# Performance work log

Hardware: AMD Instinct MI355X
Metric: run time of the kernel (lower is better)

The kernel has to match this reference:

```python
import jax, jax.numpy as jnp
import numpy as np

# SH constants (standard 3DGS eval_sh, degree 3)
C0 = 0.28209479177387814
C1 = 0.4886025119029199
C2 = (1.0925484305920792, -1.0925484305920792, 0.31539156525252005, -1.0925484305920792, 0.5462742152960396)
C3 = (-0.5900435899266435, 2.890611442640554, -0.4570457994644658, 0.3731763325901154, -0.4570457994644658, 1.445305721320277, -0.5900435899266435)

N_GAUSS = 4096
N_PTS = 32768
CHUNK = 4096  # math-identical to torch's 16384 chunking (pure concat of independent points)


def quat_to_rot(q):
    # q: (N,4) normalized, (w,x,y,z) as in 3DGS build_rotation
    r, x, y, z = q[:, 0], q[:, 1], q[:, 2], q[:, 3]
    R = jnp.stack([
        jnp.stack([1 - 2 * (y * y + z * z), 2 * (x * y - r * z), 2 * (x * z + r * y)], -1),
        jnp.stack([2 * (x * y + r * z), 1 - 2 * (x * x + z * z), 2 * (y * z - r * x)], -1),
        jnp.stack([2 * (x * z - r * y), 2 * (y * z + r * x), 1 - 2 * (x * x + y * y)], -1),
    ], axis=-2)  # (N,3,3)
    return R


def eval_sh3(sh, dirs):
    # sh: (N,16) scalar SH coeffs; dirs: (C,N,3) unit directions -> (C,N)
    x, y, z = dirs[..., 0], dirs[..., 1], dirs[..., 2]
    xx, yy, zz = x * x, y * y, z * z
    xy, yz, xz = x * y, y * z, x * z
    s = sh[None]  # (1,N,16)
    res = C0 * s[..., 0]
    res = res - C1 * y * s[..., 1] + C1 * z * s[..., 2] - C1 * x * s[..., 3]
    res = (res + C2[0] * xy * s[..., 4] + C2[1] * yz * s[..., 5]
           + C2[2] * (2 * zz - xx - yy) * s[..., 6]
           + C2[3] * xz * s[..., 7] + C2[4] * (xx - yy) * s[..., 8])
    res = (res + C3[0] * y * (3 * xx - yy) * s[..., 9] + C3[1] * xy * z * s[..., 10]
           + C3[2] * y * (4 * zz - xx - yy) * s[..., 11]
           + C3[3] * z * (2 * zz - 3 * xx - 3 * yy) * s[..., 12]
           + C3[4] * x * (4 * zz - xx - yy) * s[..., 13]
           + C3[5] * z * (xx - yy) * s[..., 14]
           + C3[6] * x * (xx - yy - 3 * zz) * s[..., 15])
    return res


def setup_inputs() -> dict:
    key = jax.random.key(0)
    ks = jax.random.split(key, 9)
    return {
        "network_pts": jax.random.normal(ks[0], (N_PTS, 3), jnp.float32),
        "network_view": jax.random.normal(ks[1], (N_PTS, 3), jnp.float32),
        "network_tx": jax.random.normal(ks[2], (N_PTS, 3), jnp.float32),
        "xyz": jax.random.normal(ks[3], (N_GAUSS, 3), jnp.float32),
        "sh_dc": jax.random.normal(ks[4], (N_GAUSS, 1), jnp.float32),
        "sh_rest": 0.1 * jax.random.normal(ks[5], (N_GAUSS, 15), jnp.float32),
        "scaling": jnp.float32(-3.0) + 0.2 * jax.random.normal(ks[6], (N_GAUSS, 3), jnp.float32),
        "rotation": jax.random.normal(ks[7], (N_GAUSS, 4), jnp.float32),
        "opacity_logit": jax.random.normal(ks[8], (N_GAUSS, 1), jnp.float32),
    }


def reference(network_pts, network_view, network_tx, xyz, sh_dc, sh_rest, scaling, rotation, opacity_logit):
    # activations, matching GaussianModel.setup_functions
    sh = jnp.concatenate([sh_dc, sh_rest], axis=1)            # (N,16)
    s = jnp.exp(scaling)                                      # (N,3)
    q = rotation / jnp.linalg.norm(rotation, axis=1, keepdims=True)
    R = quat_to_rot(q)                                        # (N,3,3)
    # precision = (L L^T)^{-1} with L = R diag(s)  =>  R diag(1/s^2) R^T
    prec = jnp.einsum('nij,nj,nkj->nik', R, 1.0 / (s * s), R)  # (N,3,3)
    op = jax.nn.sigmoid(opacity_logit)[:, 0]                  # (N,)

    pts = network_pts.reshape(-1, CHUNK, 3)

    def chunk_fn(p):  # p: (C,3)
        diff = p[:, None, :] - xyz[None, :, :]                # (C,N,3)
        maha = jnp.einsum('cni,nij,cnj->cn', diff, prec, diff)
        w = op[None, :] * jnp.exp(-0.5 * maha)                # (C,N)
        # dir_pp = xyz - query_point, normalized (as in get_magnitude)
        dirs = -diff / jnp.linalg.norm(diff, axis=-1, keepdims=True)
        mag = jnp.maximum(eval_sh3(sh, dirs), 0.0)            # (C,N)
        return w.sum(axis=1), (w * mag).sum(axis=1)

    opac_c, sig_c = jax.lax.map(chunk_fn, pts)
    return opac_c.reshape(-1), sig_c.reshape(-1)
```

## Files before the change

kernel.cpp:

```cpp
#include <hip/hip_runtime.h>
#include <hip/hip_bf16.h>

#define N_GAUSS 4096
#define N_PTS   32768
#define BLOCK   256
#define NSPLIT  32
#define SEGSZ   (N_GAUSS / NSPLIT)
#define NBLK_PT 128
#define GSTRIDE 28
#define NCELL   4096

#define SH_C0  0.28209479177387814f
#define SH_C1  0.4886025119029199f

#define WS_GP     0
#define WS_GHIST  114688
#define WS_CELLID 118784
#define WS_SPTS   151552
#define WS_PART   282624

__device__ __forceinline__ int cell_of(float x, float y, float z) {
    int cx = min(15, max(0, (int)((x + 3.2f) * 2.5f)));
    int cy = min(15, max(0, (int)((y + 3.2f) * 2.5f)));
    int cz = min(15, max(0, (int)((z + 3.2f) * 2.5f)));
    int ex = (cx & 1) | ((cx & 2) << 2) | ((cx & 4) << 4) | ((cx & 8) << 6);
    int ey = (cy & 1) | ((cy & 2) << 2) | ((cy & 4) << 4) | ((cy & 8) << 6);
    int ez = (cz & 1) | ((cz & 2) << 2) | ((cz & 4) << 4) | ((cz & 8) << 6);
    return ex | (ey << 1) | (ez << 2);
}

__global__ __launch_bounds__(1024) void setup_kernel(
    const float* __restrict__ pts, const float* __restrict__ xyz,
    const float* __restrict__ sh_dc, const float* __restrict__ sh_rest,
    const float* __restrict__ scaling, const float* __restrict__ rotation,
    const float* __restrict__ opl, float* __restrict__ gp,
    int* __restrict__ cellid, int* __restrict__ ghist)
{
    const int t = threadIdx.x, bx = blockIdx.x;

    if (bx > 0) {
        int g = (bx - 1) * 1024 + t;
        float s0 = scaling[3*g+0], s1 = scaling[3*g+1], s2 = scaling[3*g+2];
        float i0 = __expf(-2.0f * s0);
        float i1 = __expf(-2.0f * s1);
        float i2 = __expf(-2.0f * s2);
        float maxs2 = __expf(2.0f * fmaxf(s0, fmaxf(s1, s2)));

        float r = rotation[4*g+0], x = rotation[4*g+1];
        float y = rotation[4*g+2], z = rotation[4*g+3];
        float n = rsqrtf(r*r + x*x + y*y + z*z);
        r *= n; x *= n; y *= n; z *= n;
        float R00 = 1.f - 2.f*(y*y + z*z), R01 = 2.f*(x*y - r*z), R02 = 2.f*(x*z + r*y);
        float R10 = 2.f*(x*y + r*z), R11 = 1.f - 2.f*(x*x + z*z), R12 = 2.f*(y*z - r*x);
        float R20 = 2.f*(x*z - r*y), R21 = 2.f*(y*z + r*x), R22 = 1.f - 2.f*(x*x + y*y);

        float pxx = 0.5f*(R00*R00*i0 + R01*R01*i1 + R02*R02*i2);
        float pxy = 0.5f*(R00*R10*i0 + R01*R11*i1 + R02*R12*i2);
        float pxz = 0.5f*(R00*R20*i0 + R01*R21*i1 + R02*R22*i2);
        float pyy = 0.5f*(R10*R10*i0 + R11*R11*i1 + R12*R12*i2);
        float pyz = 0.5f*(R10*R20*i0 + R11*R21*i1 + R12*R22*i2);
        float pzz = 0.5f*(R20*R20*i0 + R21*R21*i1 + R22*R22*i2);

        float op   = 1.f / (1.f + __expf(-opl[g]));
        float lnop = __logf(op);
        float Tg   = 2.0f * maxs2 * (lnop + 16.0f);

        float* G = gp + (size_t)g * GSTRIDE;
        G[0] = xyz[3*g+0]; G[1] = xyz[3*g+1]; G[2] = xyz[3*g+2]; G[3] = Tg;
        G[4] = pxx; G[5] = pxy; G[6] = pxz; G[7] = pyy; G[8] = pyz; G[9] = pzz;
        G[10] = lnop; G[11] = 0.f;

        const float* sr = sh_rest + (size_t)g * 15;
        G[12] =  SH_C0 * sh_dc[g];
        G[13] = -SH_C1 * sr[0];
        G[14] =  SH_C1 * sr[1];
        G[15] = -SH_C1 * sr[2];
        G[16] =  1.0925484305920792f  * sr[3];
        G[17] = -1.0925484305920792f  * sr[4];
        G[18] =  0.31539156525252005f * sr[5];
        G[19] = -1.0925484305920792f  * sr[6];
        G[20] =  0.5462742152960396f  * sr[7];
        G[21] = -0.5900435899266435f  * sr[8];
        G[22] =  2.890611442640554f   * sr[9];
        G[23] = -0.4570457994644658f  * sr[10];
        G[24] =  0.3731763325901154f  * sr[11];
        G[25] = -0.4570457994644658f  * sr[12];
        G[26] =  1.445305721320277f   * sr[13];
        G[27] = -0.5900435899266435f  * sr[14];
        return;
    }

    __shared__ int s_hist[NCELL];
    __shared__ int s_scan[1024];
    #pragma unroll
    for (int i = 0; i < 4; ++i) s_hist[t + i * 1024] = 0;
    __syncthreads();
    for (int p = t; p < N_PTS; p += 1024) {
        float x = pts[3*p+0], y = pts[3*p+1], z = pts[3*p+2];
        int cell = cell_of(x, y, z);
        cellid[p] = cell;
        atomicAdd(&s_hist[cell], 1);
    }
    __syncthreads();
    int b = t * 4;
    int c0 = s_hist[b], c1 = s_hist[b+1], c2 = s_hist[b+2], c3 = s_hist[b+3];
    int s = c0 + c1 + c2 + c3;
    s_scan[t] = s;
    __syncthreads();
    for (int off = 1; off < 1024; off <<= 1) {
        int v = (t >= off) ? s_scan[t - off] : 0;
        __syncthreads();
        s_scan[t] += v;
        __syncthreads();
    }
    int excl = s_scan[t] - s;
    ghist[b]   = excl;
    ghist[b+1] = excl + c0;
    ghist[b+2] = excl + c0 + c1;
    ghist[b+3] = excl + c0 + c1 + c2;
}

__global__ __launch_bounds__(256) void scatter_kernel(
    const float* __restrict__ pts, const int* __restrict__ cellid,
    int* __restrict__ ghist, float4* __restrict__ spts)
{
    int p = blockIdx.x * 256 + threadIdx.x;
    float x = pts[3*p+0], y = pts[3*p+1], z = pts[3*p+2];
    int pos = atomicAdd(&ghist[cellid[p]], 1);
    spts[pos] = make_float4(x, y, z, __int_as_float(p));
}

__device__ __forceinline__ void eval_one(
    const float* __restrict__ G, float dx, float dy, float dz, float d2,
    float& opac, float& sig)
{
    float vx = G[4]*dx + G[5]*dy + G[6]*dz;
    float vy = G[5]*dx + G[7]*dy + G[8]*dz;
    float vz = G[6]*dx + G[8]*dy + G[9]*dz;
    float maha = dx*vx + dy*vy + dz*vz;
    float w = __expf(G[10] - maha);
    opac += w;

    if (__any(w > 1e-9f)) {
        float rinv = rsqrtf(d2);
        float x = -dx * rinv, y = -dy * rinv, z = -dz * rinv;
        float xx = x*x, yy = y*y, zz = z*z;
        float xy = x*y, yz = y*z, xz = x*z;

        float res = G[12];
        res += y * G[13];
        res += z * G[14];
        res += x * G[15];
        res += xy * G[16];
        res += yz * G[17];
        res += (3.f*zz - 1.f) * G[18];
        res += xz * G[19];
        float xxmyy = xx - yy;
        res += xxmyy * G[20];
        res += y * (3.f*xx - yy) * G[21];
        res += (xy * z) * G[22];
        float f5z1 = 5.f*zz - 1.f;
        res += y * f5z1 * G[23];
        res += z * (5.f*zz - 3.f) * G[24];
        res += x * f5z1 * G[25];
        res += z * xxmyy * G[26];
        res += x * (xxmyy - 3.f*zz) * G[27];

        sig += w * fmaxf(res, 0.f);
    }
}

__global__ __launch_bounds__(BLOCK, 4) void gauss_kernel(
    const float4* __restrict__ spts, const float* __restrict__ gp,
    float2* __restrict__ part)
{
    __shared__ float s_min[4][3], s_max[4][3];
    __shared__ int s_nact;
    __shared__ int s_act[SEGSZ];

    const int tid = threadIdx.x;
    const int pb  = blockIdx.x;
    const int seg = blockIdx.y;
    float4 P = spts[pb * 256 + tid];
    const float px = P.x, py = P.y, pz = P.z;

    float mnx = px, mxx = px, mny = py, mxy = py, mnz = pz, mxz = pz;
    #pragma unroll
    for (int off = 32; off >= 1; off >>= 1) {
        mnx = fminf(mnx, __shfl_xor(mnx, off));
        mxx = fmaxf(mxx, __shfl_xor(mxx, off));
        mny = fminf(mny, __shfl_xor(mny, off));
        mxy = fmaxf(mxy, __shfl_xor(mxy, off));
        mnz = fminf(mnz, __shfl_xor(mnz, off));
        mxz = fmaxf(mxz, __shfl_xor(mxz, off));
    }
    const int wave = tid >> 6;
    if ((tid & 63) == 0) {
        s_min[wave][0] = mnx; s_min[wave][1] = mny; s_min[wave][2] = mnz;
        s_max[wave][0] = mxx; s_max[wave][1] = mxy; s_max[wave][2] = mxz;
    }
    if (tid == 0) s_nact = 0;
    __syncthreads();
    const float bmnx = fminf(fminf(s_min[0][0], s_min[1][0]), fminf(s_min[2][0], s_min[3][0]));
    const float bmny = fminf(fminf(s_min[0][1], s_min[1][1]), fminf(s_min[2][1], s_min[3][1]));
    const float bmnz = fminf(fminf(s_min[0][2], s_min[1][2]), fminf(s_min[2][2], s_min[3][2]));
    const float bmxx = fmaxf(fmaxf(s_max[0][0], s_max[1][0]), fmaxf(s_max[2][0], s_max[3][0]));
    const float bmxy = fmaxf(fmaxf(s_max[0][1], s_max[1][1]), fmaxf(s_max[2][1], s_max[3][1]));
    const float bmxz = fmaxf(fmaxf(s_max[0][2], s_max[1][2]), fmaxf(s_max[2][2], s_max[3][2]));

    if (tid < SEGSZ) {
        const int gg = seg * SEGSZ + tid;
        const float* Gc = gp + (size_t)gg * GSTRIDE;
        float cx = Gc[0], cy = Gc[1], cz = Gc[2], Tg = Gc[3];
        float ddx = fmaxf(0.f, fmaxf(bmnx - cx, cx - bmxx));
        float ddy = fmaxf(0.f, fmaxf(bmny - cy, cy - bmxy));
        float ddz = fmaxf(0.f, fmaxf(bmnz - cz, cz - bmxz));
        float dd2 = ddx*ddx + ddy*ddy + ddz*ddz;
        if (dd2 <= Tg) {
            int slot = atomicAdd(&s_nact, 1);
            s_act[slot] = gg;
        }
    }
    __syncthreads();
    const int nact = s_nact;

    float opac = 0.f, sig = 0.f;
    for (int j = 0; j < nact; j += 2) {
        const bool has1 = (j + 1 < nact);
        const int g0 = __builtin_amdgcn_readfirstlane(s_act[j]);
        const int g1 = __builtin_amdgcn_readfirstlane(s_act[has1 ? j + 1 : j]);
        const float* __restrict__ A = gp + (size_t)g0 * GSTRIDE;
        const float* __restrict__ B = gp + (size_t)g1 * GSTRIDE;

        float a0 = A[0], a1 = A[1], a2 = A[2], aT = A[3];
        float b0 = B[0], b1 = B[1], b2 = B[2], bT = B[3];
        float adx = px - a0, ady = py - a1, adz = pz - a2;
        float bdx = px - b0, bdy = py - b1, bdz = pz - b2;
        float ad2 = adx*adx + ady*ady + adz*adz;
        float bd2 = bdx*bdx + bdy*bdy + bdz*bdz;

        if (!__all(ad2 > aT)) eval_one(A, adx, ady, adz, ad2, opac, sig);
        if (has1 && !__all(bd2 > bT)) eval_one(B, bdx, bdy, bdz, bd2, opac, sig);
    }

    part[((size_t)(pb * NSPLIT + seg)) * 256 + tid] = make_float2(opac, sig);
}

__global__ __launch_bounds__(256) void reduce_kernel(
    const float2* __restrict__ part, const float4* __restrict__ spts,
    float* __restrict__ out)
{
    const int tid = threadIdx.x, pb = blockIdx.x;
    float o = 0.f, sg = 0.f;
    #pragma unroll
    for (int s = 0; s < NSPLIT; ++s) {
        float2 v = part[((size_t)(pb * NSPLIT + s)) * 256 + tid];
        o += v.x; sg += v.y;
    }
    int orig = __float_as_int(spts[pb * 256 + tid].w);
    out[orig] = o;
    out[N_PTS + orig] = sg;
}

extern "C" void kernel_launch(void* const* d_in, const int* in_sizes, int n_in,
                              void* d_out, int out_size, void* d_ws, size_t ws_size,
                              hipStream_t stream) {
    const float* pts      = (const float*)d_in[0];
    const float* xyz      = (const float*)d_in[3];
    const float* sh_dc    = (const float*)d_in[4];
    const float* sh_rest  = (const float*)d_in[5];
    const float* scaling  = (const float*)d_in[6];
    const float* rotation = (const float*)d_in[7];
    const float* opl      = (const float*)d_in[8];

    float*  out    = (float*)d_out;
    float*  wsf    = (float*)d_ws;
    float*  gp     = wsf + WS_GP;
    int*    ghist  = (int*)(wsf + WS_GHIST);
    int*    cellid = (int*)(wsf + WS_CELLID);
    float4* spts   = (float4*)(wsf + WS_SPTS);
    float2* part   = (float2*)(wsf + WS_PART);

    setup_kernel<<<dim3(5), dim3(1024), 0, stream>>>(
        pts, xyz, sh_dc, sh_rest, scaling, rotation, opl, gp, cellid, ghist);
    scatter_kernel<<<dim3(NBLK_PT), dim3(256), 0, stream>>>(pts, cellid, ghist, spts);

    dim3 grid(NBLK_PT, NSPLIT);
    gauss_kernel<<<grid, dim3(BLOCK), 0, stream>>>(spts, gp, part);
    reduce_kernel<<<dim3(NBLK_PT), dim3(256), 0, stream>>>(part, spts, out);
}
```

Before: 134.3 us.

## Replace partial-sum buffer with atomic accumulation and double Gaussian splits

Gauss blocks now atomically add their per-point opacity and signal into a zeroed accumulator instead of writing per-split partials for a separate reduction. That allows the split count to grow from 32 to 64 segments for more parallelism, and blocks with no active Gaussians exit early without writing anything. Setup gets two extra blocks to zero the accumulator, and the final kernel only scatters values back to the original point order. In exchange, float atomics make the summation order nondeterministic and add atomic traffic.

```diff
diff --git a/kernel.cpp b/kernel.cpp
--- a/kernel.cpp
+++ b/kernel.cpp
@@ -4,7 +4,7 @@
 #define N_GAUSS 4096
 #define N_PTS   32768
 #define BLOCK   256
-#define NSPLIT  32
+#define NSPLIT  64
 #define SEGSZ   (N_GAUSS / NSPLIT)
 #define NBLK_PT 128
 #define GSTRIDE 28
@@ -17,7 +17,7 @@
 #define WS_GHIST  114688
 #define WS_CELLID 118784
 #define WS_SPTS   151552
-#define WS_PART   282624
+#define WS_ACC    282624
 
 __device__ __forceinline__ int cell_of(float x, float y, float z) {
     int cx = min(15, max(0, (int)((x + 3.2f) * 2.5f)));
@@ -34,10 +34,17 @@
     const float* __restrict__ sh_dc, const float* __restrict__ sh_rest,
     const float* __restrict__ scaling, const float* __restrict__ rotation,
     const float* __restrict__ opl, float* __restrict__ gp,
-    int* __restrict__ cellid, int* __restrict__ ghist)
+    int* __restrict__ cellid, int* __restrict__ ghist, float* __restrict__ acc)
 {
     const int t = threadIdx.x, bx = blockIdx.x;
 
+    if (bx >= 5) {
+        float4* a4 = (float4*)acc;
+        int base = (bx - 5) * 1024 * 8 + t;
+        #pragma unroll
+        for (int i = 0; i < 8; ++i) a4[base + i * 1024] = make_float4(0.f, 0.f, 0.f, 0.f);
+        return;
+    }
     if (bx > 0) {
         int g = (bx - 1) * 1024 + t;
         float s0 = scaling[3*g+0], s1 = scaling[3*g+1], s2 = scaling[3*g+2];
@@ -172,7 +179,7 @@
 
 __global__ __launch_bounds__(BLOCK, 4) void gauss_kernel(
     const float4* __restrict__ spts, const float* __restrict__ gp,
-    float2* __restrict__ part)
+    float* __restrict__ acc)
 {
     __shared__ float s_min[4][3], s_max[4][3];
     __shared__ int s_nact;
@@ -223,6 +230,7 @@
     }
     __syncthreads();
     const int nact = s_nact;
+    if (nact == 0) return;
 
     float opac = 0.f, sig = 0.f;
     for (int j = 0; j < nact; j += 2) {
@@ -243,23 +251,19 @@
         if (has1 && !__all(bd2 > bT)) eval_one(B, bdx, bdy, bdz, bd2, opac, sig);
     }
 
-    part[((size_t)(pb * NSPLIT + seg)) * 256 + tid] = make_float2(opac, sig);
-}
-
-__global__ __launch_bounds__(256) void reduce_kernel(
-    const float2* __restrict__ part, const float4* __restrict__ spts,
+    const int pos = pb * 256 + tid;
+    atomicAdd(&acc[pos], opac);
+    atomicAdd(&acc[N_PTS + pos], sig);
+}
+
+__global__ __launch_bounds__(256) void permute_kernel(
+    const float* __restrict__ acc, const float4* __restrict__ spts,
     float* __restrict__ out)
 {
-    const int tid = threadIdx.x, pb = blockIdx.x;
-    float o = 0.f, sg = 0.f;
-    #pragma unroll
-    for (int s = 0; s < NSPLIT; ++s) {
-        float2 v = part[((size_t)(pb * NSPLIT + s)) * 256 + tid];
-        o += v.x; sg += v.y;
-    }
-    int orig = __float_as_int(spts[pb * 256 + tid].w);
-    out[orig] = o;
-    out[N_PTS + orig] = sg;
+    int p = blockIdx.x * 256 + threadIdx.x;
+    int orig = __float_as_int(spts[p].w);
+    out[orig] = acc[p];
+    out[N_PTS + orig] = acc[N_PTS + p];
 }
 
 extern "C" void kernel_launch(void* const* d_in, const int* in_sizes, int n_in,
@@ -279,13 +283,13 @@
     int*    ghist  = (int*)(wsf + WS_GHIST);
     int*    cellid = (int*)(wsf + WS_CELLID);
     float4* spts   = (float4*)(wsf + WS_SPTS);
-    float2* part   = (float2*)(wsf + WS_PART);
-
-    setup_kernel<<<dim3(5), dim3(1024), 0, stream>>>(
-        pts, xyz, sh_dc, sh_rest, scaling, rotation, opl, gp, cellid, ghist);
+    float*  acc    = wsf + WS_ACC;
+
+    setup_kernel<<<dim3(7), dim3(1024), 0, stream>>>(
+        pts, xyz, sh_dc, sh_rest, scaling, rotation, opl, gp, cellid, ghist, acc);
     scatter_kernel<<<dim3(NBLK_PT), dim3(256), 0, stream>>>(pts, cellid, ghist, spts);
 
     dim3 grid(NBLK_PT, NSPLIT);
-    gauss_kernel<<<grid, dim3(BLOCK), 0, stream>>>(spts, gp, part);
-    reduce_kernel<<<dim3(NBLK_PT), dim3(256), 0, stream>>>(part, spts, out);
-}
+    gauss_kernel<<<grid, dim3(BLOCK), 0, stream>>>(spts, gp, acc);
+    permute_kernel<<<dim3(NBLK_PT), dim3(256), 0, stream>>>(acc, spts, out);
+}
```

New measurement: 128.6 us. -4.2%, faster.
